# Kernel optimization log

Measured on AMD Instinct MI355X. Metric: run time of the kernel, lower is better.

The kernel has to match this reference:

```python
import jax, jax.numpy as jnp
import numpy as np

N_HEADS = 4
LN_EPS = 1e-3  # keras LayerNormalization default epsilon


def setup_inputs() -> dict:
    key = jax.random.key(0)
    ks = jax.random.split(key, 9)
    B, S, D = 4, 2048, 128
    w = 0.08  # ~glorot scale for D=128
    return {
        "x": jax.random.normal(ks[0], (B, S, D), jnp.float32),
        "Wq": jax.random.normal(ks[1], (D, D), jnp.float32) * w,
        "bq": jnp.zeros((D,), jnp.float32),
        "Wk": jax.random.normal(ks[2], (D, D), jnp.float32) * w,
        "bk": jnp.zeros((D,), jnp.float32),
        "Wv": jax.random.normal(ks[3], (D, D), jnp.float32) * w,
        "bv": jnp.zeros((D,), jnp.float32),
        "Wu": jax.random.normal(ks[4], (D, 2 * D), jnp.float32) * w,
        "bu": jnp.zeros((2 * D,), jnp.float32),
        "pos_w": jax.random.normal(ks[5], (2 * S - 1,), jnp.float32) * 0.02,
        "ln_gamma": 1.0 + jax.random.normal(ks[6], (2 * D,), jnp.float32) * 0.3,
        "ln_beta": jax.random.normal(ks[7], (2 * D,), jnp.float32) * 1e-4,
        "Wf": jax.random.normal(ks[8], (2 * D, D), jnp.float32) * w,
        "bf": jnp.zeros((D,), jnp.float32),
    }


def reference(x, Wq, bq, Wk, bk, Wv, bv, Wu, bu, pos_w, ln_gamma, ln_beta, Wf, bf):
    B, S, D = x.shape
    H = N_HEADS
    hd = D // H

    # q/k/v DNNs: single Dense with silu activation (activations=["silu"])
    q = jax.nn.silu(x @ Wq + bq)
    k = jax.nn.silu(x @ Wk + bk)
    v = jax.nn.silu(x @ Wv + bv)
    u = x @ Wu + bu  # [B,S,2D], u_proj has no activation

    # relative position bias: bias[i, j] = pos_w[(S-1) + j - i]  (offset = 0)
    idx = (S - 1) + jnp.arange(S)[None, :] - jnp.arange(S)[:, None]
    rel = pos_w[idx]  # [S, S]
    pos_attn = jnp.einsum('nm,bmd->bnd', rel, v)  # [B,S,D]

    # multi-head self-attention with squared-masked-SiLU scores
    qh = q.reshape(B, S, H, hd).transpose(0, 2, 1, 3)
    kh = k.reshape(B, S, H, hd).transpose(0, 2, 1, 3)
    vh = v.reshape(B, S, H, hd).transpose(0, 2, 1, 3)
    scores = jnp.einsum('bhnd,bhmd->bhnm', qh, kh) / jnp.sqrt(jnp.float32(hd))
    causal = jnp.tril(jnp.ones((S, S), dtype=bool))  # band_part(-1, 0)
    # original: scores *= where(mask==1, scores, 0)  ->  scores^2 inside mask, 0 outside
    scores = jnp.where(causal[None, None], scores * scores, 0.0)
    self_attn = jnp.einsum('bhnm,bhmd->bhnd', jax.nn.silu(scores), vh)
    self_attn = self_attn.transpose(0, 2, 1, 3).reshape(B, S, D)

    a = jnp.concatenate([self_attn, pos_attn], axis=-1)  # [B,S,2D]
    mu = jnp.mean(a, axis=-1, keepdims=True)
    var = jnp.mean(jnp.square(a - mu), axis=-1, keepdims=True)
    a = (a - mu) * jax.lax.rsqrt(var + LN_EPS) * ln_gamma + ln_beta

    out = jax.nn.relu((u * a) @ Wf + bf) + x
    return out
```

## Files before the change

kernel.cpp:

```cpp
#include <hip/hip_runtime.h>
#include <hip/hip_bf16.h>

#define B 4
#define S 2048
#define D 128
#define H 4
#define HD 32
#define D2 256
#define BSD (B*S*D)

#define LDK 40
#define LDV 72
#define LDSC 72
#define LDX 136
#define LDH 264

typedef __attribute__((ext_vector_type(8))) short bf16x8;
typedef __attribute__((ext_vector_type(4))) short bf16x4;
typedef __attribute__((ext_vector_type(4))) float f32x4;

__device__ __forceinline__ float silu_f(float z){ return z / (1.f + __expf(-z)); }
__device__ __forceinline__ short f2bfs(float f){
    __hip_bfloat16 h = __float2bfloat16(f);
    return *reinterpret_cast<short*>(&h);
}
__device__ __forceinline__ float bfs2f(short s){
    __hip_bfloat16 h = *reinterpret_cast<__hip_bfloat16*>(&s);
    return __bfloat162float(h);
}

__global__ __launch_bounds__(256) void k_wt(
    const float* __restrict__ Wq, const float* __restrict__ Wk,
    const float* __restrict__ Wv, const float* __restrict__ Wu,
    const float* __restrict__ Wf,
    short* __restrict__ wqt, short* __restrict__ wkt, short* __restrict__ wvt,
    short* __restrict__ wut, short* __restrict__ wft)
{
    int e = blockIdx.x * 256 + threadIdx.x;
    if (e < 16384) { int n = e >> 7, k = e & 127; wqt[e] = f2bfs(Wq[k * D  + n]); return; }
    e -= 16384;
    if (e < 16384) { int n = e >> 7, k = e & 127; wkt[e] = f2bfs(Wk[k * D  + n]); return; }
    e -= 16384;
    if (e < 16384) { int n = e >> 7, k = e & 127; wvt[e] = f2bfs(Wv[k * D  + n]); return; }
    e -= 16384;
    if (e < 32768) { int n = e >> 7, k = e & 127; wut[e] = f2bfs(Wu[k * D2 + n]); return; }
    e -= 32768;
    { int n = e >> 8, k = e & 255; wft[e] = f2bfs(Wf[k * D + n]); }
}

__global__ __launch_bounds__(256) void k_qkvu(
    const float* __restrict__ x,
    const short* __restrict__ wqt, const short* __restrict__ wkt,
    const short* __restrict__ wvt, const short* __restrict__ wut,
    const float* __restrict__ bq, const float* __restrict__ bk,
    const float* __restrict__ bv, const float* __restrict__ bu,
    short* __restrict__ qb, short* __restrict__ kb, short* __restrict__ vtb,
    short* __restrict__ ub)
{
    __shared__ short xs[16 * LDX] __attribute__((aligned(16)));
    const int row0 = blockIdx.x * 16;
    const int by   = blockIdx.y;
    const int tid  = threadIdx.x;
    const int w    = tid >> 6;
    const int lane = tid & 63;
    const int q16  = lane >> 4;
    const int l15  = lane & 15;

    #pragma unroll
    for (int i = 0; i < 2; ++i) {
        int quad = tid + i * 256;
        int row = quad >> 5, c4 = (quad & 31) * 4;
        f32x4 xv = *(const f32x4*)(x + (row0 + row) * D + c4);
        short tmp[4];
        #pragma unroll
        for (int j = 0; j < 4; ++j) tmp[j] = f2bfs(xv[j]);
        *(bf16x4*)(xs + row * LDX + c4) = *(bf16x4*)tmp;
    }
    __syncthreads();

    bf16x8 af[4];
    #pragma unroll
    for (int ks = 0; ks < 4; ++ks)
        af[ks] = *(const bf16x8*)(xs + l15 * LDX + ks * 32 + q16 * 8);

    const int bb   = row0 / S;
    const int mloc = (row0 % S) + q16 * 4;

    #pragma unroll
    for (int t = 0; t < 5; ++t) {
        const int g = by * 320 + w * 80 + t * 16;
        const short* WT; const float* bias; int base; int kind;
        if (g < 128)      { WT = wqt; bias = bq; base = 0;   kind = 0; }
        else if (g < 256) { WT = wkt; bias = bk; base = 128; kind = 1; }
        else if (g < 384) { WT = wvt; bias = bv; base = 256; kind = 2; }
        else              { WT = wut; bias = bu; base = 384; kind = 3; }
        const int nloc = g - base;
        f32x4 acc = {0.f, 0.f, 0.f, 0.f};
        #pragma unroll
        for (int ks = 0; ks < 4; ++ks) {
            bf16x8 bfr = *(const bf16x8*)(WT + (nloc + l15) * D + ks * 32 + q16 * 8);
            acc = __builtin_amdgcn_mfma_f32_16x16x32_bf16(af[ks], bfr, acc, 0, 0, 0);
        }
        const float bcol = bias[nloc + l15];
        if (kind == 2) {
            short tmp[4];
            #pragma unroll
            for (int r = 0; r < 4; ++r) tmp[r] = f2bfs(silu_f(acc[r] + bcol));
            *(bf16x4*)(vtb + (bb * D + nloc + l15) * S + mloc) = *(bf16x4*)tmp;
        } else if (kind == 3) {
            #pragma unroll
            for (int r = 0; r < 4; ++r)
                ub[(row0 + q16 * 4 + r) * D2 + nloc + l15] = f2bfs(acc[r] + bcol);
        } else {
            short* dst = (kind == 0) ? qb : kb;
            #pragma unroll
            for (int r = 0; r < 4; ++r)
                dst[(row0 + q16 * 4 + r) * D + nloc + l15] = f2bfs(silu_f(acc[r] + bcol));
        }
    }
}

__global__ __launch_bounds__(256) void k_mix(
    const short* __restrict__ qb, const short* __restrict__ kb,
    const short* __restrict__ vtb, const float* __restrict__ pos_w,
    short* __restrict__ as_part, short* __restrict__ ap)
{
    __shared__ char smem[22656] __attribute__((aligned(16)));
    const int tid  = threadIdx.x;
    const int w    = tid >> 6;
    const int lane = tid & 63;
    const int q16  = lane >> 4;
    const int l15  = lane & 15;
    const int bid  = blockIdx.x;

    if (bid < 1024) {
        short* ks  = (short*)smem;
        short* vt  = (short*)(smem + 5120);
        short* scw = (short*)(smem + 9728) + w * 16 * LDSC;
        const int att = bid;
        const int nt  = 31 - (att >> 5);
        const int sub = att & 31;
        const int h   = sub & 3;
        const int b   = (sub >> 2) & 3;
        const int zz  = sub >> 4;
        const int n0  = nt * 64;

        bf16x8 qfrag = *(const bf16x8*)(qb + (b * S + n0 + w * 16 + l15) * D + h * HD + q16 * 8);
        f32x4 o0 = {0.f, 0.f, 0.f, 0.f};
        f32x4 o1 = {0.f, 0.f, 0.f, 0.f};

        const int nm    = nt + 1;
        const int half1 = (nm + 1) >> 1;
        const int it_lo = zz ? half1 : 0;
        const int it_hi = zz ? nm : half1;

        const int krow = tid >> 2, kc8 = tid & 3;
        const int vd   = tid >> 3, vm8 = tid & 7;
        const short* kp_base = kb  + (b * S + krow) * D + h * HD + kc8 * 8;
        const short* vp_base = vtb + (b * D + h * HD + vd) * S + vm8 * 8;

        bf16x8 kreg = *(const bf16x8*)(kp_base + it_lo * 64 * D);
        bf16x8 vreg = *(const bf16x8*)(vp_base + it_lo * 64);

        for (int it = it_lo; it < it_hi; ++it) {
            const int m0 = it * 64;
            __syncthreads();
            *(bf16x8*)(ks + krow * LDK + kc8 * 8) = kreg;
            *(bf16x8*)(vt + vd * LDV + vm8 * 8)   = vreg;
            __syncthreads();
            if (it + 1 < it_hi) {
                kreg = *(const bf16x8*)(kp_base + (it + 1) * 64 * D);
                vreg = *(const bf16x8*)(vp_base + (it + 1) * 64);
            }
            if (it != nt) {
                #pragma unroll
                for (int t = 0; t < 4; ++t) {
                    bf16x8 kf = *(const bf16x8*)(ks + (t * 16 + l15) * LDK + q16 * 8);
                    f32x4 sacc = {0.f, 0.f, 0.f, 0.f};
                    sacc = __builtin_amdgcn_mfma_f32_16x16x32_bf16(kf, qfrag, sacc, 0, 0, 0);
                    short tmp[4];
                    #pragma unroll
                    for (int r = 0; r < 4; ++r) {
                        float sv = sacc[r] * 0.17677669529663687f;
                        tmp[r] = f2bfs(silu_f(sv * sv));
                    }
                    *(bf16x4*)(scw + l15 * LDSC + t * 16 + q16 * 4) = *(bf16x4*)tmp;
                }
            } else {
                const int query_g = n0 + w * 16 + l15;
                #pragma unroll
                for (int t = 0; t < 4; ++t) {
                    bf16x8 kf = *(const bf16x8*)(ks + (t * 16 + l15) * LDK + q16 * 8);
                    f32x4 sacc = {0.f, 0.f, 0.f, 0.f};
                    sacc = __builtin_amdgcn_mfma_f32_16x16x32_bf16(kf, qfrag, sacc, 0, 0, 0);
                    const int key_gb = m0 + t * 16 + q16 * 4;
                    short tmp[4];
                    #pragma unroll
                    for (int r = 0; r < 4; ++r) {
                        float sv = sacc[r] * 0.17677669529663687f;
                        float wgt = silu_f(sv * sv);
                        if (key_gb + r > query_g) wgt = 0.f;
                        tmp[r] = f2bfs(wgt);
                    }
                    *(bf16x4*)(scw + l15 * LDSC + t * 16 + q16 * 4) = *(bf16x4*)tmp;
                }
            }
            #pragma unroll
            for (int kt = 0; kt < 2; ++kt) {
                bf16x8 pf = *(const bf16x8*)(scw + l15 * LDSC + kt * 32 + q16 * 8);
                bf16x8 v0 = *(const bf16x8*)(vt + l15 * LDV        + kt * 32 + q16 * 8);
                bf16x8 v1 = *(const bf16x8*)(vt + (16 + l15) * LDV + kt * 32 + q16 * 8);
                o0 = __builtin_amdgcn_mfma_f32_16x16x32_bf16(pf, v0, o0, 0, 0, 0);
                o1 = __builtin_amdgcn_mfma_f32_16x16x32_bf16(pf, v1, o1, 0, 0, 0);
            }
        }
        short* dst = as_part + zz * BSD;
        const int nrow = n0 + w * 16 + q16 * 4;
        #pragma unroll
        for (int r = 0; r < 4; ++r) {
            dst[(b * S + nrow + r) * D + h * HD + l15]      = f2bfs(o0[r]);
            dst[(b * S + nrow + r) * D + h * HD + 16 + l15] = f2bfs(o1[r]);
        }
    } else {
        float* pwf = (float*)smem;
        short* vt  = (short*)(smem + 4224);
        const int pid = bid - 1024;
        const int n0  = (pid >> 3) * 32;
        const int sub = pid & 7;
        const int b   = sub >> 1;
        const int z   = sub & 1;
        const int s   = w >> 1;
        const int dh  = w & 1;

        const int base_g = 2016 + z * 1024 - n0;
        for (int i = tid; i < 1055; i += 256) pwf[i] = pos_w[base_g + i];

        f32x4 acc[4];
        #pragma unroll
        for (int dt = 0; dt < 4; ++dt) acc[dt] = (f32x4){0.f, 0.f, 0.f, 0.f};

        int sd[4], sm8[4];
        const short* vp[4];
        #pragma unroll
        for (int i = 0; i < 4; ++i) {
            int e = tid + i * 256;
            sd[i] = e >> 3; sm8[i] = e & 7;
            vp[i] = vtb + (b * D + sd[i]) * S + z * 1024 + sm8[i] * 8;
        }
        bf16x8 vreg[4];
        #pragma unroll
        for (int i = 0; i < 4; ++i) vreg[i] = *(const bf16x8*)(vp[i]);

        for (int mt = 0; mt < 16; ++mt) {
            __syncthreads();
            #pragma unroll
            for (int i = 0; i < 4; ++i)
                *(bf16x8*)(vt + sd[i] * LDV + sm8[i] * 8) = vreg[i];
            __syncthreads();
            if (mt + 1 < 16) {
                #pragma unroll
                for (int i = 0; i < 4; ++i)
                    vreg[i] = *(const bf16x8*)(vp[i] + (mt + 1) * 64);
            }
            #pragma unroll
            for (int kt = 0; kt < 2; ++kt) {
                const int idx0 = mt * 64 + kt * 32 + q16 * 8 + 31 - s * 16 - l15;
                union { unsigned int u[4]; bf16x8 v; } cvt;
                #pragma unroll
                for (int p = 0; p < 4; ++p) {
                    unsigned int a0 = __float_as_uint(pwf[idx0 + 2 * p])     + 0x8000u;
                    unsigned int a1 = __float_as_uint(pwf[idx0 + 2 * p + 1]) + 0x8000u;
                    cvt.u[p] = __builtin_amdgcn_perm(a1, a0, 0x07060302u);
                }
                bf16x8 af = cvt.v;
                #pragma unroll
                for (int dt = 0; dt < 4; ++dt) {
                    bf16x8 bv = *(const bf16x8*)(vt + (dh * 64 + dt * 16 + l15) * LDV + kt * 32 + q16 * 8);
                    acc[dt] = __builtin_amdgcn_mfma_f32_16x16x32_bf16(af, bv, acc[dt], 0, 0, 0);
                }
            }
        }
        short* dst = ap + z * BSD;
        const int nrow = n0 + s * 16 + q16 * 4;
        #pragma unroll
        for (int dt = 0; dt < 4; ++dt)
            #pragma unroll
            for (int r = 0; r < 4; ++r)
                dst[(b * S + nrow + r) * D + dh * 64 + dt * 16 + l15] = f2bfs(acc[dt][r]);
    }
}

__global__ __launch_bounds__(256) void k_final(
    const short* __restrict__ as_part, const short* __restrict__ ap,
    const short* __restrict__ ub, const short* __restrict__ wft,
    const float* __restrict__ gamma, const float* __restrict__ beta,
    const float* __restrict__ bfb,
    const float* __restrict__ x, float* __restrict__ out)
{
    __shared__ short hsb[16 * LDH] __attribute__((aligned(16)));
    const int tid  = threadIdx.x;
    const int row0 = blockIdx.x * 8;

    for (int i = tid; i < 8 * LDH; i += 256) hsb[8 * LDH + i] = 0;

    {
        const int row = tid >> 5;
        const int c   = tid & 31;
        float av[8];
        float s1 = 0.f, s2 = 0.f;
        #pragma unroll
        for (int j = 0; j < 8; ++j) {
            int col = c + j * 32;
            float v_;
            if (col < 128)
                v_ = bfs2f(as_part[(row0 + row) * D + col]) +
                     bfs2f(as_part[BSD + (row0 + row) * D + col]);
            else {
                int c2 = col - 128;
                v_ = bfs2f(ap[(row0 + row) * D + c2]) +
                     bfs2f(ap[BSD + (row0 + row) * D + c2]);
            }
            av[j] = v_;
            s1 += v_;
            s2 += v_ * v_;
        }
        #pragma unroll
        for (int off = 1; off < 32; off <<= 1) {
            s1 += __shfl_xor(s1, off);
            s2 += __shfl_xor(s2, off);
        }
        float mu  = s1 * (1.f / 256.f);
        float var = s2 * (1.f / 256.f) - mu * mu;
        float rs  = rsqrtf(var + 1e-3f);
        #pragma unroll
        for (int j = 0; j < 8; ++j) {
            int col = c + j * 32;
            float an = (av[j] - mu) * rs * gamma[col] + beta[col];
            float h  = bfs2f(ub[(row0 + row) * D2 + col]) * an;
            hsb[row * LDH + col] = f2bfs(h);
        }
    }
    __syncthreads();

    const int w    = tid >> 6;
    const int lane = tid & 63;
    const int q16  = lane >> 4;
    const int l15  = lane & 15;
    f32x4 o[2];
    o[0] = (f32x4){0.f, 0.f, 0.f, 0.f};
    o[1] = (f32x4){0.f, 0.f, 0.f, 0.f};
    #pragma unroll
    for (int ks = 0; ks < 8; ++ks) {
        bf16x8 af = *(const bf16x8*)(hsb + l15 * LDH + ks * 32 + q16 * 8);
        #pragma unroll
        for (int ci = 0; ci < 2; ++ci) {
            const int ct = w * 2 + ci;
            bf16x8 bfr = *(const bf16x8*)(wft + (ct * 16 + l15) * D2 + ks * 32 + q16 * 8);
            o[ci] = __builtin_amdgcn_mfma_f32_16x16x32_bf16(af, bfr, o[ci], 0, 0, 0);
        }
    }
    if (q16 < 2) {
        #pragma unroll
        for (int ci = 0; ci < 2; ++ci) {
            const int n = (w * 2 + ci) * 16 + l15;
            const float bfv = bfb[n];
            #pragma unroll
            for (int r = 0; r < 4; ++r) {
                const int row = row0 + q16 * 4 + r;
                float oo = o[ci][r] + bfv;
                oo = fmaxf(oo, 0.f);
                oo += x[row * D + n];
                out[row * D + n] = oo;
            }
        }
    }
}

extern "C" void kernel_launch(void* const* d_in, const int* in_sizes, int n_in,
                              void* d_out, int out_size, void* d_ws, size_t ws_size,
                              hipStream_t stream)
{
    const float* x     = (const float*)d_in[0];
    const float* Wq    = (const float*)d_in[1];
    const float* bq    = (const float*)d_in[2];
    const float* Wk    = (const float*)d_in[3];
    const float* bk    = (const float*)d_in[4];
    const float* Wv    = (const float*)d_in[5];
    const float* bv    = (const float*)d_in[6];
    const float* Wu    = (const float*)d_in[7];
    const float* bu    = (const float*)d_in[8];
    const float* pos_w = (const float*)d_in[9];
    const float* gamma = (const float*)d_in[10];
    const float* beta  = (const float*)d_in[11];
    const float* Wf    = (const float*)d_in[12];
    const float* bfb   = (const float*)d_in[13];
    float* out = (float*)d_out;

    char* p = (char*)d_ws;
    short* qb      = (short*)p;  p += (size_t)BSD * 2;
    short* kb      = (short*)p;  p += (size_t)BSD * 2;
    short* vtb     = (short*)p;  p += (size_t)BSD * 2;
    short* ubuf    = (short*)p;  p += (size_t)2 * BSD * 2;
    short* as_part = (short*)p;  p += (size_t)2 * BSD * 2;
    short* ap      = (short*)p;  p += (size_t)2 * BSD * 2;
    short* wqt     = (short*)p;  p += (size_t)D * D * 2;
    short* wkt     = (short*)p;  p += (size_t)D * D * 2;
    short* wvt     = (short*)p;  p += (size_t)D * D * 2;
    short* wut     = (short*)p;  p += (size_t)D2 * D * 2;
    short* wft     = (short*)p;  p += (size_t)D * D2 * 2;

    k_wt   <<<dim3(448),    256, 0, stream>>>(Wq, Wk, Wv, Wu, Wf, wqt, wkt, wvt, wut, wft);
    k_qkvu <<<dim3(512, 2), 256, 0, stream>>>(x, wqt, wkt, wvt, wut, bq, bk, bv, bu, qb, kb, vtb, ubuf);
    k_mix  <<<dim3(1536),   256, 0, stream>>>(qb, kb, vtb, pos_w, as_part, ap);
    k_final<<<dim3(1024),   256, 0, stream>>>(as_part, ap, ubuf, wft, gamma, beta, bfb, x, out);
}
```

Before: 138.6 us.

## Enlarge attention query tile to 128 rows so each K/V tile serves twice the queries

The causal attention blocks now cover 128 queries (32 per wave, two 16-row fragments) instead of 64, which halves the number of attention blocks and halves K/V tile loads per query. Each staged 64-key K/V tile feeds twice as many MFMAs, and the masking branch is chosen per wave from its query range. In exchange, register pressure rises, there are fewer blocks to balance the triangular workload, and some waves idle on the diagonal tiles where their queries are fully masked.

```diff
diff --git a/kernel.cpp b/kernel.cpp
--- a/kernel.cpp
+++ b/kernel.cpp
@@ -125,7 +125,7 @@
     const short* __restrict__ vtb, const float* __restrict__ pos_w,
     short* __restrict__ as_part, short* __restrict__ ap)
 {
-    __shared__ char smem[22656] __attribute__((aligned(16)));
+    __shared__ char smem[28160] __attribute__((aligned(16)));
     const int tid  = threadIdx.x;
     const int w    = tid >> 6;
     const int lane = tid & 63;
@@ -133,26 +133,30 @@
     const int l15  = lane & 15;
     const int bid  = blockIdx.x;
 
-    if (bid < 1024) {
+    if (bid < 512) {
         short* ks  = (short*)smem;
         short* vt  = (short*)(smem + 5120);
-        short* scw = (short*)(smem + 9728) + w * 16 * LDSC;
+        short* scw = (short*)(smem + 9728) + w * 32 * LDSC;
         const int att = bid;
-        const int nt  = 31 - (att >> 5);
+        const int nt  = 15 - (att >> 5);
         const int sub = att & 31;
         const int h   = sub & 3;
         const int b   = (sub >> 2) & 3;
         const int zz  = sub >> 4;
-        const int n0  = nt * 64;
-
-        bf16x8 qfrag = *(const bf16x8*)(qb + (b * S + n0 + w * 16 + l15) * D + h * HD + q16 * 8);
-        f32x4 o0 = {0.f, 0.f, 0.f, 0.f};
-        f32x4 o1 = {0.f, 0.f, 0.f, 0.f};
-
-        const int nm    = nt + 1;
-        const int half1 = (nm + 1) >> 1;
+        const int n0  = nt * 128;
+
+        bf16x8 qf0 = *(const bf16x8*)(qb + (b * S + n0 + w * 32 + l15) * D + h * HD + q16 * 8);
+        bf16x8 qf1 = *(const bf16x8*)(qb + (b * S + n0 + w * 32 + 16 + l15) * D + h * HD + q16 * 8);
+        f32x4 o00 = {0.f,0.f,0.f,0.f}, o01 = {0.f,0.f,0.f,0.f};
+        f32x4 o10 = {0.f,0.f,0.f,0.f}, o11 = {0.f,0.f,0.f,0.f};
+
+        const int nm    = 2 * nt + 2;
+        const int half1 = nt + 1;
         const int it_lo = zz ? half1 : 0;
         const int it_hi = zz ? nm : half1;
+
+        const int wq_min = n0 + w * 32;
+        const int wq_max = wq_min + 31;
 
         const int krow = tid >> 2, kc8 = tid & 3;
         const int vd   = tid >> 3, vm8 = tid & 7;
@@ -172,59 +176,79 @@
                 kreg = *(const bf16x8*)(kp_base + (it + 1) * 64 * D);
                 vreg = *(const bf16x8*)(vp_base + (it + 1) * 64);
             }
-            if (it != nt) {
+            if (m0 <= wq_max) {
+                if (m0 + 63 <= wq_min) {
+                    #pragma unroll
+                    for (int t = 0; t < 4; ++t) {
+                        bf16x8 kf = *(const bf16x8*)(ks + (t * 16 + l15) * LDK + q16 * 8);
+                        f32x4 s0 = {0.f,0.f,0.f,0.f};
+                        f32x4 s1 = {0.f,0.f,0.f,0.f};
+                        s0 = __builtin_amdgcn_mfma_f32_16x16x32_bf16(kf, qf0, s0, 0, 0, 0);
+                        s1 = __builtin_amdgcn_mfma_f32_16x16x32_bf16(kf, qf1, s1, 0, 0, 0);
+                        short t0[4], t1[4];
+                        #pragma unroll
+                        for (int r = 0; r < 4; ++r) {
+                            float a0 = s0[r] * 0.17677669529663687f;
+                            float a1 = s1[r] * 0.17677669529663687f;
+                            t0[r] = f2bfs(silu_f(a0 * a0));
+                            t1[r] = f2bfs(silu_f(a1 * a1));
+                        }
+                        *(bf16x4*)(scw + l15 * LDSC        + t * 16 + q16 * 4) = *(bf16x4*)t0;
+                        *(bf16x4*)(scw + (16 + l15) * LDSC + t * 16 + q16 * 4) = *(bf16x4*)t1;
+                    }
+                } else {
+                    const int qg0 = wq_min + l15;
+                    const int qg1 = wq_min + 16 + l15;
+                    #pragma unroll
+                    for (int t = 0; t < 4; ++t) {
+                        bf16x8 kf = *(const bf16x8*)(ks + (t * 16 + l15) * LDK + q16 * 8);
+                        f32x4 s0 = {0.f,0.f,0.f,0.f};
+                        f32x4 s1 = {0.f,0.f,0.f,0.f};
+                        s0 = __builtin_amdgcn_mfma_f32_16x16x32_bf16(kf, qf0, s0, 0, 0, 0);
+                        s1 = __builtin_amdgcn_mfma_f32_16x16x32_bf16(kf, qf1, s1, 0, 0, 0);
+                        const int key_gb = m0 + t * 16 + q16 * 4;
+                        short t0[4], t1[4];
+                        #pragma unroll
+                        for (int r = 0; r < 4; ++r) {
+                            float a0 = s0[r] * 0.17677669529663687f;
+                            float a1 = s1[r] * 0.17677669529663687f;
+                            float w0 = silu_f(a0 * a0);
+                            float w1 = silu_f(a1 * a1);
+                            if (key_gb + r > qg0) w0 = 0.f;
+                            if (key_gb + r > qg1) w1 = 0.f;
+                            t0[r] = f2bfs(w0);
+                            t1[r] = f2bfs(w1);
+                        }
+                        *(bf16x4*)(scw + l15 * LDSC        + t * 16 + q16 * 4) = *(bf16x4*)t0;
+                        *(bf16x4*)(scw + (16 + l15) * LDSC + t * 16 + q16 * 4) = *(bf16x4*)t1;
+                    }
+                }
                 #pragma unroll
-                for (int t = 0; t < 4; ++t) {
-                    bf16x8 kf = *(const bf16x8*)(ks + (t * 16 + l15) * LDK + q16 * 8);
-                    f32x4 sacc = {0.f, 0.f, 0.f, 0.f};
-                    sacc = __builtin_amdgcn_mfma_f32_16x16x32_bf16(kf, qfrag, sacc, 0, 0, 0);
-                    short tmp[4];
-                    #pragma unroll
-                    for (int r = 0; r < 4; ++r) {
-                        float sv = sacc[r] * 0.17677669529663687f;
-                        tmp[r] = f2bfs(silu_f(sv * sv));
-                    }
-                    *(bf16x4*)(scw + l15 * LDSC + t * 16 + q16 * 4) = *(bf16x4*)tmp;
+                for (int kt = 0; kt < 2; ++kt) {
+                    bf16x8 pf0 = *(const bf16x8*)(scw + l15 * LDSC        + kt * 32 + q16 * 8);
+                    bf16x8 pf1 = *(const bf16x8*)(scw + (16 + l15) * LDSC + kt * 32 + q16 * 8);
+                    bf16x8 v0  = *(const bf16x8*)(vt + l15 * LDV        + kt * 32 + q16 * 8);
+                    bf16x8 v1  = *(const bf16x8*)(vt + (16 + l15) * LDV + kt * 32 + q16 * 8);
+                    o00 = __builtin_amdgcn_mfma_f32_16x16x32_bf16(pf0, v0, o00, 0, 0, 0);
+                    o01 = __builtin_amdgcn_mfma_f32_16x16x32_bf16(pf0, v1, o01, 0, 0, 0);
+                    o10 = __builtin_amdgcn_mfma_f32_16x16x32_bf16(pf1, v0, o10, 0, 0, 0);
+                    o11 = __builtin_amdgcn_mfma_f32_16x16x32_bf16(pf1, v1, o11, 0, 0, 0);
                 }
-            } else {
-                const int query_g = n0 + w * 16 + l15;
-                #pragma unroll
-                for (int t = 0; t < 4; ++t) {
-                    bf16x8 kf = *(const bf16x8*)(ks + (t * 16 + l15) * LDK + q16 * 8);
-                    f32x4 sacc = {0.f, 0.f, 0.f, 0.f};
-                    sacc = __builtin_amdgcn_mfma_f32_16x16x32_bf16(kf, qfrag, sacc, 0, 0, 0);
-                    const int key_gb = m0 + t * 16 + q16 * 4;
-                    short tmp[4];
-                    #pragma unroll
-                    for (int r = 0; r < 4; ++r) {
-                        float sv = sacc[r] * 0.17677669529663687f;
-                        float wgt = silu_f(sv * sv);
-                        if (key_gb + r > query_g) wgt = 0.f;
-                        tmp[r] = f2bfs(wgt);
-                    }
-                    *(bf16x4*)(scw + l15 * LDSC + t * 16 + q16 * 4) = *(bf16x4*)tmp;
-                }
-            }
-            #pragma unroll
-            for (int kt = 0; kt < 2; ++kt) {
-                bf16x8 pf = *(const bf16x8*)(scw + l15 * LDSC + kt * 32 + q16 * 8);
-                bf16x8 v0 = *(const bf16x8*)(vt + l15 * LDV        + kt * 32 + q16 * 8);
-                bf16x8 v1 = *(const bf16x8*)(vt + (16 + l15) * LDV + kt * 32 + q16 * 8);
-                o0 = __builtin_amdgcn_mfma_f32_16x16x32_bf16(pf, v0, o0, 0, 0, 0);
-                o1 = __builtin_amdgcn_mfma_f32_16x16x32_bf16(pf, v1, o1, 0, 0, 0);
             }
         }
         short* dst = as_part + zz * BSD;
-        const int nrow = n0 + w * 16 + q16 * 4;
+        const int nrow0 = n0 + w * 32 + q16 * 4;
         #pragma unroll
         for (int r = 0; r < 4; ++r) {
-            dst[(b * S + nrow + r) * D + h * HD + l15]      = f2bfs(o0[r]);
-            dst[(b * S + nrow + r) * D + h * HD + 16 + l15] = f2bfs(o1[r]);
+            dst[(b * S + nrow0 + r) * D + h * HD + l15]           = f2bfs(o00[r]);
+            dst[(b * S + nrow0 + r) * D + h * HD + 16 + l15]      = f2bfs(o01[r]);
+            dst[(b * S + nrow0 + 16 + r) * D + h * HD + l15]      = f2bfs(o10[r]);
+            dst[(b * S + nrow0 + 16 + r) * D + h * HD + 16 + l15] = f2bfs(o11[r]);
         }
     } else {
         float* pwf = (float*)smem;
         short* vt  = (short*)(smem + 4224);
-        const int pid = bid - 1024;
+        const int pid = bid - 512;
         const int n0  = (pid >> 3) * 32;
         const int sub = pid & 7;
         const int b   = sub >> 1;
@@ -411,6 +435,6 @@
 
     k_wt   <<<dim3(448),    256, 0, stream>>>(Wq, Wk, Wv, Wu, Wf, wqt, wkt, wvt, wut, wft);
     k_qkvu <<<dim3(512, 2), 256, 0, stream>>>(x, wqt, wkt, wvt, wut, bq, bk, bv, bu, qb, kb, vtb, ubuf);
-    k_mix  <<<dim3(1536),   256, 0, stream>>>(qb, kb, vtb, pos_w, as_part, ap);
+    k_mix  <<<dim3(1024),   256, 0, stream>>>(qb, kb, vtb, pos_w, as_part, ap);
     k_final<<<dim3(1024),   256, 0, stream>>>(as_part, ap, ubuf, wft, gamma, beta, bfb, x, out);
 }
```

Result: slower. 147.3 us (+6.3%).
